# Optimization experiments

Hardware: AMD Instinct MI355X
Metric: run time of the kernel (lower is better)

The kernel has to match this reference:

```python
import jax, jax.numpy as jnp
import numpy as np

N = 100000      # num_edges in original graph = nodes here
E = 1600000     # edges of the line-graph
F_IN = 16       # num_edge_features
H, C = 2, 32    # heads, hidden_channels
HC = H * C
TD = 16         # time_embedding_dim
CD = 16         # condition_dim
NC = 2          # num_classes
MAX_TIME = 1000.0
THETA = 1.0


def _glorot(key, shape):
    fan_in = shape[0]
    return jax.random.normal(key, shape, dtype=jnp.float32) / np.sqrt(fan_in)


def setup_inputs() -> dict:
    key = jax.random.key(0)
    ks = jax.random.split(key, 32)
    inp = {
        "x": jax.random.normal(ks[0], (N, F_IN), dtype=jnp.float32),
        "edge_index": jax.random.randint(ks[1], (2, E), 0, N, dtype=jnp.int64),
        "t": jax.random.randint(ks[2], (1,), 0, 1000, dtype=jnp.int64),
        "condition": jax.random.normal(ks[3], (N, CD), dtype=jnp.float32),
        # GATv2 layer 0 (bias=True)
        "Wl0": _glorot(ks[4], (F_IN, HC)), "bl0": jnp.zeros((HC,), jnp.float32),
        "Wr0": _glorot(ks[5], (F_IN, HC)), "br0": jnp.zeros((HC,), jnp.float32),
        "att0": _glorot(ks[6], (H, C)), "bias0": jnp.zeros((HC,), jnp.float32),
        "Wres0": _glorot(ks[7], (F_IN, HC)), "bres0": jnp.zeros((HC,), jnp.float32),
        # GATv2 layer 1 (bias=False)
        "Wl1": _glorot(ks[8], (HC, HC)),
        "Wr1": _glorot(ks[9], (HC, HC)),
        "att1": _glorot(ks[10], (H, C)),
        "Wres1": _glorot(ks[11], (HC, HC)), "bres1": jnp.zeros((HC,), jnp.float32),
        # time MLP
        "Wt0": _glorot(ks[12], (TD, TD)), "bt0": jnp.zeros((TD,), jnp.float32),
        "Wt1": _glorot(ks[13], (TD, TD)), "bt1": jnp.zeros((TD,), jnp.float32),
        # decoder heads
        "Wfd": _glorot(ks[14], (HC + CD + TD, C)), "bfd": jnp.zeros((C,), jnp.float32),
        "Wcls": _glorot(ks[15], (C, NC)), "bcls": jnp.zeros((NC,), jnp.float32),
    }
    return inp


def _segment_softmax(logits, seg, num_seg):
    # logits: [E, H], softmax over edges sharing the same destination node
    m = jax.ops.segment_max(logits, seg, num_segments=num_seg)
    ex = jnp.exp(logits - m[seg])
    s = jax.ops.segment_sum(ex, seg, num_segments=num_seg)
    return ex / (s[seg] + 1e-16)


def _gatv2(x, src, dst, Wl, bl, Wr, br, att, bias):
    # PyG GATv2Conv with add_self_loops (self loops appended by caller)
    xl = x @ Wl
    xr = x @ Wr
    if bl is not None:
        xl = xl + bl
        xr = xr + br
    xl = xl.reshape(-1, H, C)
    xr = xr.reshape(-1, H, C)
    e = jax.nn.leaky_relu(xl[src] + xr[dst], negative_slope=0.2)  # [E, H, C]
    logits = jnp.einsum('ehc,hc->eh', e, att)                     # [E, H]
    alpha = _segment_softmax(logits, dst, N)                      # [E, H]
    msg = xl[src] * alpha[:, :, None]                             # [E, H, C]
    out = jax.ops.segment_sum(msg, dst, num_segments=N)           # [N, H, C]
    out = out.reshape(N, HC)
    if bias is not None:
        out = out + bias
    return out


def _time_embedding(t):
    tf = t.astype(jnp.float32) * (1000.0 / MAX_TIME)
    half = TD // 2
    freqs = jnp.exp(jnp.arange(half, dtype=jnp.float32) * -(jnp.log(10000.0) / (half - 1)))
    ang = tf[:, None] * freqs[None, :]
    return jnp.concatenate([jnp.sin(ang), jnp.cos(ang)], axis=1)  # [1, TD]


def reference(x, edge_index, t, condition,
              Wl0, bl0, Wr0, br0, att0, bias0, Wres0, bres0,
              Wl1, Wr1, att1, Wres1, bres1,
              Wt0, bt0, Wt1, bt1, Wfd, bfd, Wcls, bcls):
    loops = jnp.arange(N, dtype=edge_index.dtype)
    src = jnp.concatenate([edge_index[0], loops])
    dst = jnp.concatenate([edge_index[1], loops])

    # layer 0
    res = jax.nn.relu(x @ Wres0 + bres0)
    h = jax.nn.relu(_gatv2(x, src, dst, Wl0, bl0, Wr0, br0, att0, bias0))
    h = THETA * h + res
    # layer 1 (bias=False)
    res = jax.nn.relu(h @ Wres1 + bres1)
    h2 = jax.nn.relu(_gatv2(h, src, dst, Wl1, None, Wr1, None, att1, None))
    h = THETA * h2 + res

    # mode == 'future'
    t_emb = _time_embedding(t)
    t_emb = jax.nn.silu(t_emb @ Wt0 + bt0)
    t_emb = jax.nn.silu(t_emb @ Wt1 + bt1)
    t_rep = jnp.tile(t_emb, (N, 1))                                # [N, TD]
    h = jnp.concatenate([h, t_rep, condition], axis=1)             # [N, HC+TD+CD]
    logits = h @ Wfd + bfd
    logits = logits @ Wcls + bcls
    return logits[None]                                            # [1, N, NC]
```

## Files before the change

### kernel.cpp

```cpp
#include <hip/hip_runtime.h>
#include <hip/hip_bf16.h>
#include <hip/hip_fp16.h>
#include <math.h>


#define BLK 256
#define BDST 32
#define CDST 256
#define CHUNK 4096
#define FCAP 768
#define NBC_MAX 512

typedef _Float16 half4v __attribute__((ext_vector_type(4)));
typedef _Float16 half2v __attribute__((ext_vector_type(2)));

#if __has_builtin(__builtin_amdgcn_fdot2)
#define FDOT2(a, b, c) __builtin_amdgcn_fdot2((a), (b), (c), false)
#else
__device__ __forceinline__ float fdot2_fallback(half2v a, half2v b, float c) {
    return c + (float)a.x * (float)b.x + (float)a.y * (float)b.y;
}
#define FDOT2(a, b, c) fdot2_fallback((a), (b), (c))
#endif

__device__ __forceinline__ float leaky02(float x) { return x >= 0.f ? x : 0.2f * x; }
__device__ __forceinline__ float relu(float x) { return x > 0.f ? x : 0.f; }

__device__ __forceinline__ float edot(half4v h, half2v xlo, half2v xhi,
                                      half2v alo, half2v ahi, half2v c02) {
    half2v lo = half2v{h.x, h.y} + xlo;
    half2v hi = half2v{h.z, h.w} + xhi;
    lo = __builtin_elementwise_max(lo, lo * c02);
    hi = __builtin_elementwise_max(hi, hi * c02);
    return FDOT2(lo, alo, FDOT2(hi, ahi, 0.f));
}

__global__ void k_tiny(const int* __restrict__ t,
                       const float* __restrict__ Wt0, const float* __restrict__ bt0,
                       const float* __restrict__ Wt1, const float* __restrict__ bt1,
                       const float* __restrict__ Wfd, const float* __restrict__ bfd,
                       const float* __restrict__ Wcls, const float* __restrict__ bcls,
                       float* __restrict__ wcomb,
                       float* __restrict__ bfinal)
{
    __shared__ float temb[16];
    int tid = threadIdx.x;
    if (tid == 0) {
        float tf = (float)t[0];
        float e0[16], v1[16];
        const float cexp = -logf(10000.f) / 7.f;
        for (int j = 0; j < 8; ++j) {
            float ang = tf * expf((float)j * cexp);
            e0[j] = sinf(ang);
            e0[8 + j] = cosf(ang);
        }
        for (int i = 0; i < 16; ++i) {
            float a = bt0[i];
            for (int j = 0; j < 16; ++j) a += e0[j] * Wt0[j * 16 + i];
            v1[i] = a / (1.f + expf(-a));
        }
        for (int i = 0; i < 16; ++i) {
            float a = bt1[i];
            for (int j = 0; j < 16; ++j) a += v1[j] * Wt1[j * 16 + i];
            temb[i] = a / (1.f + expf(-a));
        }
    }
    __syncthreads();
    if (tid < 192) {
        int i = tid >> 1, k = tid & 1;
        float a = 0.f;
        for (int j = 0; j < 32; ++j) a += Wfd[i * 32 + j] * Wcls[j * 2 + k];
        wcomb[tid] = a;
    }
    __syncthreads();
    if (tid < 2) {
        float a = bcls[tid];
        for (int j = 0; j < 32; ++j) a += bfd[j] * Wcls[j * 2 + tid];
        for (int d = 0; d < 16; ++d) a += temb[d] * wcomb[(64 + d) * 2 + tid];
        bfinal[tid] = a;
    }
}

__global__ void k_zeroc(int* __restrict__ ccnt, int NBC)
{
    int gid = blockIdx.x * BLK + threadIdx.x;
    if (gid < NBC) ccnt[gid] = 0;
}

__global__ void k_histc(const int* __restrict__ ei, int E, int NBC,
                        int* __restrict__ ccnt)
{
    __shared__ int h[NBC_MAX];
    int tid = threadIdx.x;
    for (int i = tid; i < NBC; i += BLK) h[i] = 0;
    __syncthreads();
    int e0 = blockIdx.x * CHUNK;
    #pragma unroll
    for (int k = 0; k < CHUNK / BLK; ++k) {
        int e = e0 + tid + k * BLK;
        if (e < E) atomicAdd(&h[ei[E + e] >> 8], 1);
    }
    __syncthreads();
    for (int i = tid; i < NBC; i += BLK) {
        int v = h[i];
        if (v) atomicAdd(&ccnt[i], v);
    }
}

__global__ void k_scan(const int* __restrict__ ccnt, int NBC, int E,
                       int* __restrict__ cbase, int* __restrict__ ccur)
{
    if (threadIdx.x == 0) {
        int acc = 0;
        for (int i = 0; i < NBC; ++i) {
            cbase[i] = acc;
            acc += ccnt[i];
        }
        cbase[NBC] = acc;
    }
    __syncthreads();
    for (int i = threadIdx.x; i < NBC; i += BLK) ccur[i] = cbase[i];
}

__global__ void k_part(const int* __restrict__ ei, int E, int NBC,
                       int* __restrict__ ccur, int* __restrict__ part)
{
    __shared__ int h[NBC_MAX];
    __shared__ int gb[NBC_MAX];
    int tid = threadIdx.x;
    int e0 = blockIdx.x * CHUNK;
    for (int i = tid; i < NBC; i += BLK) h[i] = 0;
    __syncthreads();
    int sv[CHUNK / BLK], dv[CHUNK / BLK];
    #pragma unroll
    for (int k = 0; k < CHUNK / BLK; ++k) {
        int e = e0 + tid + k * BLK;
        if (e < E) {
            sv[k] = ei[e];
            dv[k] = ei[E + e];
            atomicAdd(&h[dv[k] >> 8], 1);
        } else dv[k] = -1;
    }
    __syncthreads();
    for (int i = tid; i < NBC; i += BLK) {
        int v = h[i];
        gb[i] = v ? atomicAdd(&ccur[i], v) : 0;
    }
    __syncthreads();
    for (int i = tid; i < NBC; i += BLK) h[i] = gb[i];
    __syncthreads();
    #pragma unroll
    for (int k = 0; k < CHUNK / BLK; ++k) {
        if (dv[k] >= 0) {
            int p = atomicAdd(&h[dv[k] >> 8], 1);
            part[p] = (sv[k] << 8) | (dv[k] & 255);
        }
    }
}

__global__ void k_refine(const int* __restrict__ cbase, const int* __restrict__ part,
                         int NBF, int* __restrict__ fbeg, int* __restrict__ fend,
                         int* __restrict__ srcs)
{
    __shared__ int fcnt[8];
    __shared__ int fcur[8];
    int b = blockIdx.x, tid = threadIdx.x;
    int beg = cbase[b], end = cbase[b + 1];
    if (tid < 8) fcnt[tid] = 0;
    __syncthreads();
    for (int k = beg + tid; k < end; k += BLK)
        atomicAdd(&fcnt[(part[k] >> 5) & 7], 1);
    __syncthreads();
    if (tid == 0) {
        int acc = beg;
        #pragma unroll
        for (int f = 0; f < 8; ++f) {
            int fb = b * 8 + f;
            fcur[f] = acc;
            if (fb < NBF) { fbeg[fb] = acc; acc += fcnt[f]; fend[fb] = acc; }
        }
    }
    __syncthreads();
    for (int k = beg + tid; k < end; k += BLK) {
        int tg = part[k];
        int p = atomicAdd(&fcur[(tg >> 5) & 7], 1);
        srcs[p] = ((tg >> 8) << 5) | (tg & 31);
    }
}

__global__ void k_pre0f(const float* __restrict__ x,
                        const float* __restrict__ Wl, const float* __restrict__ bl,
                        const float* __restrict__ Wr, const float* __restrict__ br,
                        const float* __restrict__ Wres, const float* __restrict__ bres,
                        _Float16* __restrict__ xlh, _Float16* __restrict__ xr16,
                        _Float16* __restrict__ res16, int N)
{
    int wid = (int)(((long long)blockIdx.x * BLK + threadIdx.x) >> 6);
    int lane = threadIdx.x & 63;
    int g = lane >> 4, q = lane & 15;
    int n = wid * 4 + g;
    bool valid = n < N;
    int nn = valid ? n : N - 1;
    float xv = x[(size_t)nn * 16 + q];
    int c0 = q * 4;
    float4 accl = *(const float4*)(bl + c0);
    float4 accr = *(const float4*)(br + c0);
    float4 accs = *(const float4*)(bres + c0);
    #pragma unroll
    for (int k = 0; k < 16; ++k) {
        float xk = __shfl(xv, (g << 4) | k, 64);
        float4 wl = *(const float4*)(Wl + k * 64 + c0);
        float4 wr = *(const float4*)(Wr + k * 64 + c0);
        float4 wsv = *(const float4*)(Wres + k * 64 + c0);
        accl.x = fmaf(xk, wl.x, accl.x);
        accl.y = fmaf(xk, wl.y, accl.y);
        accl.z = fmaf(xk, wl.z, accl.z);
        accl.w = fmaf(xk, wl.w, accl.w);
        accr.x = fmaf(xk, wr.x, accr.x);
        accr.y = fmaf(xk, wr.y, accr.y);
        accr.z = fmaf(xk, wr.z, accr.z);
        accr.w = fmaf(xk, wr.w, accr.w);
        accs.x = fmaf(xk, wsv.x, accs.x);
        accs.y = fmaf(xk, wsv.y, accs.y);
        accs.z = fmaf(xk, wsv.z, accs.z);
        accs.w = fmaf(xk, wsv.w, accs.w);
    }
    if (valid) {
        size_t base = (size_t)n * 64 + c0;
        half4v hl, hr, hs;
        hl.x = (_Float16)accl.x; hl.y = (_Float16)accl.y;
        hl.z = (_Float16)accl.z; hl.w = (_Float16)accl.w;
        hr.x = (_Float16)accr.x; hr.y = (_Float16)accr.y;
        hr.z = (_Float16)accr.z; hr.w = (_Float16)accr.w;
        hs.x = (_Float16)relu(accs.x); hs.y = (_Float16)relu(accs.y);
        hs.z = (_Float16)relu(accs.z); hs.w = (_Float16)relu(accs.w);
        *(half4v*)(xlh + base) = hl;
        *(half4v*)(xr16 + base) = hr;
        *(half4v*)(res16 + base) = hs;
    }
}

__global__ void k_pre1w(const _Float16* __restrict__ h16,
                        const float* __restrict__ Wl, const float* __restrict__ Wr,
                        const float* __restrict__ Wres, const float* __restrict__ bres,
                        _Float16* __restrict__ xlh, _Float16* __restrict__ xr16,
                        _Float16* __restrict__ res16, int N)
{
    __shared__ half4v wl4[16][64];
    __shared__ half4v wr4[16][64];
    __shared__ half4v ws4[16][64];
    __shared__ half4v h4[32][16];
    int tid = threadIdx.x;
    int nb = blockIdx.x * 32;

    for (int idx = tid; idx < 3 * 1024; idx += BLK) {
        int m = idx >> 10, rem = idx & 1023;
        int k4 = rem >> 6, c = rem & 63;
        const float* W = (m == 0) ? Wl : (m == 1) ? Wr : Wres;
        half4v v;
        v.x = (_Float16)W[(4 * k4 + 0) * 64 + c];
        v.y = (_Float16)W[(4 * k4 + 1) * 64 + c];
        v.z = (_Float16)W[(4 * k4 + 2) * 64 + c];
        v.w = (_Float16)W[(4 * k4 + 3) * 64 + c];
        (m == 0 ? wl4 : m == 1 ? wr4 : ws4)[k4][c] = v;
    }
    for (int idx = tid; idx < 512; idx += BLK) {
        int i = idx >> 4, k4 = idx & 15;
        int n = nb + i; if (n >= N) n = N - 1;
        h4[i][k4] = *(const half4v*)(h16 + (size_t)n * 64 + k4 * 4);
    }
    __syncthreads();

    int c = tid & 63, w = tid >> 6;
    float al[8], ar[8], as[8];
    float vbs = bres[c];
    #pragma unroll
    for (int i = 0; i < 8; ++i) { al[i] = 0.f; ar[i] = 0.f; as[i] = vbs; }

    #pragma unroll 4
    for (int k4 = 0; k4 < 16; ++k4) {
        half4v wl = wl4[k4][c];
        half4v wr = wr4[k4][c];
        half4v wsv = ws4[k4][c];
        half2v wll = { wl.x, wl.y },  wlh = { wl.z, wl.w };
        half2v wrl = { wr.x, wr.y },  wrh = { wr.z, wr.w };
        half2v wsl = { wsv.x, wsv.y }, wsh = { wsv.z, wsv.w };
        #pragma unroll
        for (int i = 0; i < 8; ++i) {
            half4v hv = h4[w * 8 + i][k4];
            half2v hl = { hv.x, hv.y }, hh = { hv.z, hv.w };
            al[i] = FDOT2(hl, wll, al[i]);
            al[i] = FDOT2(hh, wlh, al[i]);
            ar[i] = FDOT2(hl, wrl, ar[i]);
            ar[i] = FDOT2(hh, wrh, ar[i]);
            as[i] = FDOT2(hl, wsl, as[i]);
            as[i] = FDOT2(hh, wsh, as[i]);
        }
    }
    #pragma unroll
    for (int i = 0; i < 8; ++i) {
        int n = nb + w * 8 + i;
        if (n < N) {
            xlh[(size_t)n * 64 + c]   = (_Float16)al[i];
            xr16[(size_t)n * 64 + c]  = (_Float16)ar[i];
            res16[(size_t)n * 64 + c] = (_Float16)relu(as[i]);
        }
    }
}

template <bool DEC>
__global__ void k_gat3(const int* __restrict__ fbeg, const int* __restrict__ fend,
                       const int* __restrict__ srcs,
                       const _Float16* __restrict__ xlh, const _Float16* __restrict__ xr16,
                       const float* __restrict__ att, const float* __restrict__ bias,
                       const _Float16* __restrict__ res16,
                       _Float16* __restrict__ hout16,
                       const float* __restrict__ cond, const float* __restrict__ wcomb,
                       const float* __restrict__ bfinal, float* __restrict__ out,
                       int N)
{
    __shared__ int lh[BDST];
    __shared__ int rp[BDST + 1];
    __shared__ int cc[BDST];
    __shared__ int sidx[BDST];
    __shared__ int tags[FCAP];

    int b = blockIdx.x;
    int tid = threadIdx.x;
    int beg = fbeg[b];
    int nE = fend[b] - beg; if (nE > FCAP) nE = FCAP;

    if (tid < BDST) lh[tid] = 0;
    __syncthreads();
    for (int k = tid; k < nE; k += BLK) atomicAdd(&lh[srcs[beg + k] & 31], 1);
    __syncthreads();
    if (tid == 0) {
        int acc = 0;
        rp[0] = 0;
        #pragma unroll
        for (int i = 0; i < BDST; ++i) { acc += lh[i]; rp[i + 1] = acc; }
    }
    __syncthreads();
    if (tid < BDST) cc[tid] = rp[tid];
    __syncthreads();
    for (int k = tid; k < nE; k += BLK) {
        int tg = srcs[beg + k];
        int r = atomicAdd(&cc[tg & 31], 1);
        tags[r] = tg >> 5;
    }
    if (tid < BDST) {
        int di = rp[tid + 1] - rp[tid];
        int r = 0;
        #pragma unroll
        for (int j = 0; j < BDST; ++j) {
            int dj = rp[j + 1] - rp[j];
            r += (dj > di) || (dj == di && j < tid);
        }
        sidx[r] = tid;
    }
    __syncthreads();

    int lane = tid & 63, w = tid >> 6;
    int g = lane >> 4, q = lane & 15;
    int c0 = q * 4;
    float4 a4f = *(const float4*)(att + c0);
    const half2v c02 = { (_Float16)0.2f, (_Float16)0.2f };
    half2v alo = { (_Float16)a4f.x, (_Float16)a4f.y };
    half2v ahi = { (_Float16)a4f.z, (_Float16)a4f.w };

    #pragma unroll
    for (int rep = 0; rep < 2; ++rep) {
        int dlow = sidx[w * 8 + rep * 4 + g];
        int node = b * BDST + dlow;
        bool nvalid = node < N;
        int n = nvalid ? node : 0;

        half4v xrh = *(const half4v*)(xr16 + (size_t)n * 64 + c0);
        half2v xlo = { xrh.x, xrh.y }, xhi = { xrh.z, xrh.w };

        half4v hsv = *(const half4v*)(xlh + (size_t)n * 64 + c0);
        float lv = edot(hsv, xlo, xhi, alo, ahi, c02);
        lv += __shfl_xor(lv, 1, 8);
        lv += __shfl_xor(lv, 2, 8);
        lv += __shfl_xor(lv, 4, 8);

        float m = lv, den = 1.f;
        float ac0 = (float)hsv.x, ac1 = (float)hsv.y;
        float ac2 = (float)hsv.z, ac3 = (float)hsv.w;

        int deg = nvalid ? (rp[dlow + 1] - rp[dlow]) : 0;
        int base = nvalid ? rp[dlow] : 0;

        int t1 = max(deg, __shfl_xor(deg, 16, 64));
        int wavemax = max(t1, __shfl_xor(t1, 32, 64));

        int i1 = (0 < deg) ? tags[base + 0] : n;
        int i2 = (1 < deg) ? tags[base + 1] : n;
        int i3 = (2 < deg) ? tags[base + 2] : n;
        int i4 = (3 < deg) ? tags[base + 3] : n;
        half4v p1 = *(const half4v*)(xlh + (size_t)i1 * 64 + c0);
        half4v p2 = *(const half4v*)(xlh + (size_t)i2 * 64 + c0);
        half4v p3 = *(const half4v*)(xlh + (size_t)i3 * 64 + c0);
        half4v p4 = *(const half4v*)(xlh + (size_t)i4 * 64 + c0);

        for (int j = 0; j < wavemax; j += 4) {
            bool a1 = j < deg, a2 = j + 1 < deg, a3 = j + 2 < deg, a4b = j + 3 < deg;
            half4v h1 = p1, h2 = p2, h3 = p3, h4 = p4;
            int n1 = (j + 4 < deg) ? tags[base + j + 4] : n;
            int n2 = (j + 5 < deg) ? tags[base + j + 5] : n;
            int n3 = (j + 6 < deg) ? tags[base + j + 6] : n;
            int n4 = (j + 7 < deg) ? tags[base + j + 7] : n;
            p1 = *(const half4v*)(xlh + (size_t)n1 * 64 + c0);
            p2 = *(const half4v*)(xlh + (size_t)n2 * 64 + c0);
            p3 = *(const half4v*)(xlh + (size_t)n3 * 64 + c0);
            p4 = *(const half4v*)(xlh + (size_t)n4 * 64 + c0);

            float e1 = edot(h1, xlo, xhi, alo, ahi, c02);
            float e2 = edot(h2, xlo, xhi, alo, ahi, c02);
            float e3 = edot(h3, xlo, xhi, alo, ahi, c02);
            float e4 = edot(h4, xlo, xhi, alo, ahi, c02);
            e1 += __shfl_xor(e1, 1, 8); e2 += __shfl_xor(e2, 1, 8);
            e3 += __shfl_xor(e3, 1, 8); e4 += __shfl_xor(e4, 1, 8);
            e1 += __shfl_xor(e1, 2, 8); e2 += __shfl_xor(e2, 2, 8);
            e3 += __shfl_xor(e3, 2, 8); e4 += __shfl_xor(e4, 2, 8);
            e1 += __shfl_xor(e1, 4, 8); e2 += __shfl_xor(e2, 4, 8);
            e3 += __shfl_xor(e3, 4, 8); e4 += __shfl_xor(e4, 4, 8);
            if (!a1) e1 = -1e30f;
            if (!a2) e2 = -1e30f;
            if (!a3) e3 = -1e30f;
            if (!a4b) e4 = -1e30f;

            float mn = fmaxf(fmaxf(m, fmaxf(e1, e2)), fmaxf(e3, e4));
            float sc  = __expf(m - mn);
            float ex1 = __expf(e1 - mn);
            float ex2 = __expf(e2 - mn);
            float ex3 = __expf(e3 - mn);
            float ex4 = __expf(e4 - mn);
            den = den * sc + ((ex1 + ex2) + (ex3 + ex4));
            ac0 = fmaf(ex4, (float)h4.x, fmaf(ex3, (float)h3.x,
                  fmaf(ex2, (float)h2.x, fmaf(ex1, (float)h1.x, ac0 * sc))));
            ac1 = fmaf(ex4, (float)h4.y, fmaf(ex3, (float)h3.y,
                  fmaf(ex2, (float)h2.y, fmaf(ex1, (float)h1.y, ac1 * sc))));
            ac2 = fmaf(ex4, (float)h4.z, fmaf(ex3, (float)h3.z,
                  fmaf(ex2, (float)h2.z, fmaf(ex1, (float)h1.z, ac2 * sc))));
            ac3 = fmaf(ex4, (float)h4.w, fmaf(ex3, (float)h3.w,
                  fmaf(ex2, (float)h2.w, fmaf(ex1, (float)h1.w, ac3 * sc))));
            m = mn;
        }

        float inv = 1.f / den;
        half4v rh = *(const half4v*)(res16 + (size_t)n * 64 + c0);
        float h0, h1, h2, h3;
        if (bias) {
            const float4 b4 = *(const float4*)(bias + c0);
            h0 = relu(ac0 * inv + b4.x) + (float)rh.x;
            h1 = relu(ac1 * inv + b4.y) + (float)rh.y;
            h2 = relu(ac2 * inv + b4.z) + (float)rh.z;
            h3 = relu(ac3 * inv + b4.w) + (float)rh.w;
        } else {
            h0 = relu(ac0 * inv) + (float)rh.x;
            h1 = relu(ac1 * inv) + (float)rh.y;
            h2 = relu(ac2 * inv) + (float)rh.z;
            h3 = relu(ac3 * inv) + (float)rh.w;
        }

        if (!DEC) {
            if (nvalid) {
                half4v o;
                o.x = (_Float16)h0; o.y = (_Float16)h1;
                o.z = (_Float16)h2; o.w = (_Float16)h3;
                *(half4v*)(hout16 + (size_t)n * 64 + c0) = o;
            }
        } else {
            float p0 = h0 * wcomb[(c0 + 0) * 2] + h1 * wcomb[(c0 + 1) * 2]
                     + h2 * wcomb[(c0 + 2) * 2] + h3 * wcomb[(c0 + 3) * 2];
            float p1d = h0 * wcomb[(c0 + 0) * 2 + 1] + h1 * wcomb[(c0 + 1) * 2 + 1]
                      + h2 * wcomb[(c0 + 2) * 2 + 1] + h3 * wcomb[(c0 + 3) * 2 + 1];
            if (q < 4) {
                float4 c4 = *(const float4*)(cond + (size_t)n * 16 + q * 4);
                int d0 = 80 + q * 4;
                p0 += c4.x * wcomb[(d0 + 0) * 2] + c4.y * wcomb[(d0 + 1) * 2]
                    + c4.z * wcomb[(d0 + 2) * 2] + c4.w * wcomb[(d0 + 3) * 2];
                p1d += c4.x * wcomb[(d0 + 0) * 2 + 1] + c4.y * wcomb[(d0 + 1) * 2 + 1]
                     + c4.z * wcomb[(d0 + 2) * 2 + 1] + c4.w * wcomb[(d0 + 3) * 2 + 1];
            }
            #pragma unroll
            for (int off = 1; off < 16; off <<= 1) {
                p0 += __shfl_xor(p0, off, 16);
                p1d += __shfl_xor(p1d, off, 16);
            }
            if (q == 0 && nvalid) {
                out[(size_t)n * 2] = p0 + bfinal[0];
                out[(size_t)n * 2 + 1] = p1d + bfinal[1];
            }
        }
    }
}

static inline int gblk(long long threads) { return (int)((threads + BLK - 1) / BLK); }

extern "C" void kernel_launch(void* const* d_in, const int* in_sizes, int n_in,
                              void* d_out, int out_size, void* d_ws, size_t ws_size,
                              hipStream_t stream) {
    const float* x     = (const float*)d_in[0];
    const int*   ei    = (const int*)d_in[1];
    const int*   t     = (const int*)d_in[2];
    const float* cond  = (const float*)d_in[3];
    const float* Wl0   = (const float*)d_in[4];
    const float* bl0   = (const float*)d_in[5];
    const float* Wr0   = (const float*)d_in[6];
    const float* br0   = (const float*)d_in[7];
    const float* att0  = (const float*)d_in[8];
    const float* bias0 = (const float*)d_in[9];
    const float* Wres0 = (const float*)d_in[10];
    const float* bres0 = (const float*)d_in[11];
    const float* Wl1   = (const float*)d_in[12];
    const float* Wr1   = (const float*)d_in[13];
    const float* att1  = (const float*)d_in[14];
    const float* Wres1 = (const float*)d_in[15];
    const float* bres1 = (const float*)d_in[16];
    const float* Wt0   = (const float*)d_in[17];
    const float* bt0   = (const float*)d_in[18];
    const float* Wt1   = (const float*)d_in[19];
    const float* bt1   = (const float*)d_in[20];
    const float* Wfd   = (const float*)d_in[21];
    const float* bfd   = (const float*)d_in[22];
    const float* Wcls  = (const float*)d_in[23];
    const float* bcls  = (const float*)d_in[24];
    float* out = (float*)d_out;

    const int N   = in_sizes[0] / 16;
    const int E   = in_sizes[1] / 2;
    const int NBC = (N + CDST - 1) / CDST;
    const int NBF = (N + BDST - 1) / BDST;

    float* ws = (float*)d_ws;
    size_t o = 0;
    _Float16* hbuf16 = (_Float16*)(ws + o); o += (size_t)N * 32;
    _Float16* xlh    = (_Float16*)(ws + o); o += (size_t)N * 32;
    _Float16* xr16   = (_Float16*)(ws + o); o += (size_t)N * 32;
    _Float16* res16  = (_Float16*)(ws + o); o += (size_t)N * 32;
    float* wcomb = ws + o; o += 192;
    float* bfin  = ws + o; o += 2;
    int* iws     = (int*)(ws + o);
    size_t io = 0;
    int* ccnt  = iws + io; io += NBC_MAX;
    int* cbase = iws + io; io += NBC_MAX + 1;
    int* ccur  = iws + io; io += NBC_MAX;
    int* fbeg  = iws + io; io += NBF;
    int* fend  = iws + io; io += NBF;
    int* part  = iws + io; io += E;
    int* srcs  = iws + io; io += E;

    const int partBlocks = (E + CHUNK - 1) / CHUNK;

    k_tiny<<<1, BLK, 0, stream>>>(t, Wt0, bt0, Wt1, bt1, Wfd, bfd, Wcls, bcls, wcomb, bfin);

    k_zeroc<<<gblk(NBC), BLK, 0, stream>>>(ccnt, NBC);
    k_histc<<<partBlocks, BLK, 0, stream>>>(ei, E, NBC, ccnt);
    k_scan<<<1, BLK, 0, stream>>>(ccnt, NBC, E, cbase, ccur);
    k_part<<<partBlocks, BLK, 0, stream>>>(ei, E, NBC, ccur, part);
    k_refine<<<NBC, BLK, 0, stream>>>(cbase, part, NBF, fbeg, fend, srcs);

    k_pre0f<<<gblk((long long)((N + 3) / 4) * 64), BLK, 0, stream>>>(
        x, Wl0, bl0, Wr0, br0, Wres0, bres0, xlh, xr16, res16, N);
    k_gat3<false><<<NBF, BLK, 0, stream>>>(fbeg, fend, srcs, xlh, xr16, att0, bias0, res16,
                                           hbuf16, nullptr, nullptr, nullptr, nullptr, N);

    k_pre1w<<<(N + 31) / 32, BLK, 0, stream>>>(hbuf16, Wl1, Wr1, Wres1, bres1, xlh, xr16, res16, N);
    k_gat3<true><<<NBF, BLK, 0, stream>>>(fbeg, fend, srcs, xlh, xr16, att1, nullptr, res16,
                                          nullptr, cond, wcomb, bfin, out, N);
}
```

Measured before the change: 274.4 us.

## Fuse layer-1 projection GEMM into the layer-0 GAT aggregation kernel

```diff
diff --git a/kernel.cpp b/kernel.cpp
--- a/kernel.cpp
+++ b/kernel.cpp
@@ -240,81 +240,16 @@
     }
 }
 
-__global__ void k_pre1w(const _Float16* __restrict__ h16,
-                        const float* __restrict__ Wl, const float* __restrict__ Wr,
-                        const float* __restrict__ Wres, const float* __restrict__ bres,
-                        _Float16* __restrict__ xlh, _Float16* __restrict__ xr16,
-                        _Float16* __restrict__ res16, int N)
-{
-    __shared__ half4v wl4[16][64];
-    __shared__ half4v wr4[16][64];
-    __shared__ half4v ws4[16][64];
-    __shared__ half4v h4[32][16];
-    int tid = threadIdx.x;
-    int nb = blockIdx.x * 32;
-
-    for (int idx = tid; idx < 3 * 1024; idx += BLK) {
-        int m = idx >> 10, rem = idx & 1023;
-        int k4 = rem >> 6, c = rem & 63;
-        const float* W = (m == 0) ? Wl : (m == 1) ? Wr : Wres;
-        half4v v;
-        v.x = (_Float16)W[(4 * k4 + 0) * 64 + c];
-        v.y = (_Float16)W[(4 * k4 + 1) * 64 + c];
-        v.z = (_Float16)W[(4 * k4 + 2) * 64 + c];
-        v.w = (_Float16)W[(4 * k4 + 3) * 64 + c];
-        (m == 0 ? wl4 : m == 1 ? wr4 : ws4)[k4][c] = v;
-    }
-    for (int idx = tid; idx < 512; idx += BLK) {
-        int i = idx >> 4, k4 = idx & 15;
-        int n = nb + i; if (n >= N) n = N - 1;
-        h4[i][k4] = *(const half4v*)(h16 + (size_t)n * 64 + k4 * 4);
-    }
-    __syncthreads();
-
-    int c = tid & 63, w = tid >> 6;
-    float al[8], ar[8], as[8];
-    float vbs = bres[c];
-    #pragma unroll
-    for (int i = 0; i < 8; ++i) { al[i] = 0.f; ar[i] = 0.f; as[i] = vbs; }
-
-    #pragma unroll 4
-    for (int k4 = 0; k4 < 16; ++k4) {
-        half4v wl = wl4[k4][c];
-        half4v wr = wr4[k4][c];
-        half4v wsv = ws4[k4][c];
-        half2v wll = { wl.x, wl.y },  wlh = { wl.z, wl.w };
-        half2v wrl = { wr.x, wr.y },  wrh = { wr.z, wr.w };
-        half2v wsl = { wsv.x, wsv.y }, wsh = { wsv.z, wsv.w };
-        #pragma unroll
-        for (int i = 0; i < 8; ++i) {
-            half4v hv = h4[w * 8 + i][k4];
-            half2v hl = { hv.x, hv.y }, hh = { hv.z, hv.w };
-            al[i] = FDOT2(hl, wll, al[i]);
-            al[i] = FDOT2(hh, wlh, al[i]);
-            ar[i] = FDOT2(hl, wrl, ar[i]);
-            ar[i] = FDOT2(hh, wrh, ar[i]);
-            as[i] = FDOT2(hl, wsl, as[i]);
-            as[i] = FDOT2(hh, wsh, as[i]);
-        }
-    }
-    #pragma unroll
-    for (int i = 0; i < 8; ++i) {
-        int n = nb + w * 8 + i;
-        if (n < N) {
-            xlh[(size_t)n * 64 + c]   = (_Float16)al[i];
-            xr16[(size_t)n * 64 + c]  = (_Float16)ar[i];
-            res16[(size_t)n * 64 + c] = (_Float16)relu(as[i]);
-        }
-    }
-}
-
-template <bool DEC>
+template <int LAYER>
 __global__ void k_gat3(const int* __restrict__ fbeg, const int* __restrict__ fend,
                        const int* __restrict__ srcs,
                        const _Float16* __restrict__ xlh, const _Float16* __restrict__ xr16,
                        const float* __restrict__ att, const float* __restrict__ bias,
                        const _Float16* __restrict__ res16,
-                       _Float16* __restrict__ hout16,
+                       const float* __restrict__ Wl1, const float* __restrict__ Wr1,
+                       const float* __restrict__ Wres1, const float* __restrict__ bres1,
+                       _Float16* __restrict__ xlh_out, _Float16* __restrict__ xr_out,
+                       _Float16* __restrict__ res_out,
                        const float* __restrict__ cond, const float* __restrict__ wcomb,
                        const float* __restrict__ bfinal, float* __restrict__ out,
                        int N)
@@ -324,11 +259,29 @@
     __shared__ int cc[BDST];
     __shared__ int sidx[BDST];
     __shared__ int tags[FCAP];
+    __shared__ half4v wl4[LAYER == 0 ? 16 : 1][64];
+    __shared__ half4v wr4[LAYER == 0 ? 16 : 1][64];
+    __shared__ half4v ws4[LAYER == 0 ? 16 : 1][64];
+    __shared__ half4v h4[LAYER == 0 ? 32 : 1][16];
 
     int b = blockIdx.x;
     int tid = threadIdx.x;
     int beg = fbeg[b];
     int nE = fend[b] - beg; if (nE > FCAP) nE = FCAP;
+
+    if constexpr (LAYER == 0) {
+        for (int idx = tid; idx < 3 * 1024; idx += BLK) {
+            int m = idx >> 10, rem = idx & 1023;
+            int k4 = rem >> 6, c = rem & 63;
+            const float* W = (m == 0) ? Wl1 : (m == 1) ? Wr1 : Wres1;
+            half4v v;
+            v.x = (_Float16)W[(4 * k4 + 0) * 64 + c];
+            v.y = (_Float16)W[(4 * k4 + 1) * 64 + c];
+            v.z = (_Float16)W[(4 * k4 + 2) * 64 + c];
+            v.w = (_Float16)W[(4 * k4 + 3) * 64 + c];
+            (m == 0 ? wl4 : m == 1 ? wr4 : ws4)[k4][c] = v;
+        }
+    }
 
     if (tid < BDST) lh[tid] = 0;
     __syncthreads();
@@ -405,7 +358,7 @@
 
         for (int j = 0; j < wavemax; j += 4) {
             bool a1 = j < deg, a2 = j + 1 < deg, a3 = j + 2 < deg, a4b = j + 3 < deg;
-            half4v h1 = p1, h2 = p2, h3 = p3, h4 = p4;
+            half4v h1 = p1, h2 = p2, h3 = p3, h4x = p4;
             int n1 = (j + 4 < deg) ? tags[base + j + 4] : n;
             int n2 = (j + 5 < deg) ? tags[base + j + 5] : n;
             int n3 = (j + 6 < deg) ? tags[base + j + 6] : n;
@@ -418,7 +371,7 @@
             float e1 = edot(h1, xlo, xhi, alo, ahi, c02);
             float e2 = edot(h2, xlo, xhi, alo, ahi, c02);
             float e3 = edot(h3, xlo, xhi, alo, ahi, c02);
-            float e4 = edot(h4, xlo, xhi, alo, ahi, c02);
+            float e4 = edot(h4x, xlo, xhi, alo, ahi, c02);
             e1 += __shfl_xor(e1, 1, 8); e2 += __shfl_xor(e2, 1, 8);
             e3 += __shfl_xor(e3, 1, 8); e4 += __shfl_xor(e4, 1, 8);
             e1 += __shfl_xor(e1, 2, 8); e2 += __shfl_xor(e2, 2, 8);
@@ -437,13 +390,13 @@
             float ex3 = __expf(e3 - mn);
             float ex4 = __expf(e4 - mn);
             den = den * sc + ((ex1 + ex2) + (ex3 + ex4));
-            ac0 = fmaf(ex4, (float)h4.x, fmaf(ex3, (float)h3.x,
+            ac0 = fmaf(ex4, (float)h4x.x, fmaf(ex3, (float)h3.x,
                   fmaf(ex2, (float)h2.x, fmaf(ex1, (float)h1.x, ac0 * sc))));
-            ac1 = fmaf(ex4, (float)h4.y, fmaf(ex3, (float)h3.y,
+            ac1 = fmaf(ex4, (float)h4x.y, fmaf(ex3, (float)h3.y,
                   fmaf(ex2, (float)h2.y, fmaf(ex1, (float)h1.y, ac1 * sc))));
-            ac2 = fmaf(ex4, (float)h4.z, fmaf(ex3, (float)h3.z,
+            ac2 = fmaf(ex4, (float)h4x.z, fmaf(ex3, (float)h3.z,
                   fmaf(ex2, (float)h2.z, fmaf(ex1, (float)h1.z, ac2 * sc))));
-            ac3 = fmaf(ex4, (float)h4.w, fmaf(ex3, (float)h3.w,
+            ac3 = fmaf(ex4, (float)h4x.w, fmaf(ex3, (float)h3.w,
                   fmaf(ex2, (float)h2.w, fmaf(ex1, (float)h1.w, ac3 * sc))));
             m = mn;
         }
@@ -464,13 +417,11 @@
             h3 = relu(ac3 * inv) + (float)rh.w;
         }
 
-        if (!DEC) {
-            if (nvalid) {
-                half4v o;
-                o.x = (_Float16)h0; o.y = (_Float16)h1;
-                o.z = (_Float16)h2; o.w = (_Float16)h3;
-                *(half4v*)(hout16 + (size_t)n * 64 + c0) = o;
-            }
+        if constexpr (LAYER == 0) {
+            half4v o;
+            o.x = (_Float16)h0; o.y = (_Float16)h1;
+            o.z = (_Float16)h2; o.w = (_Float16)h3;
+            h4[dlow][q] = o;
         } else {
             float p0 = h0 * wcomb[(c0 + 0) * 2] + h1 * wcomb[(c0 + 1) * 2]
                      + h2 * wcomb[(c0 + 2) * 2] + h3 * wcomb[(c0 + 3) * 2];
@@ -492,6 +443,46 @@
             if (q == 0 && nvalid) {
                 out[(size_t)n * 2] = p0 + bfinal[0];
                 out[(size_t)n * 2 + 1] = p1d + bfinal[1];
+            }
+        }
+    }
+
+    if constexpr (LAYER == 0) {
+        __syncthreads();
+        int nb = b * BDST;
+        int c = tid & 63, ww = tid >> 6;
+        float al[8], ar[8], as2[8];
+        float vbs = bres1[c];
+        #pragma unroll
+        for (int i = 0; i < 8; ++i) { al[i] = 0.f; ar[i] = 0.f; as2[i] = vbs; }
+
+        #pragma unroll 4
+        for (int k4 = 0; k4 < 16; ++k4) {
+            half4v wl = wl4[k4][c];
+            half4v wr = wr4[k4][c];
+            half4v wsv = ws4[k4][c];
+            half2v wll = { wl.x, wl.y },  wlh = { wl.z, wl.w };
+            half2v wrl = { wr.x, wr.y },  wrh = { wr.z, wr.w };
+            half2v wsl = { wsv.x, wsv.y }, wsh = { wsv.z, wsv.w };
+            #pragma unroll
+            for (int i = 0; i < 8; ++i) {
+                half4v hv = h4[ww * 8 + i][k4];
+                half2v hl = { hv.x, hv.y }, hh = { hv.z, hv.w };
+                al[i] = FDOT2(hl, wll, al[i]);
+                al[i] = FDOT2(hh, wlh, al[i]);
+                ar[i] = FDOT2(hl, wrl, ar[i]);
+                ar[i] = FDOT2(hh, wrh, ar[i]);
+                as2[i] = FDOT2(hl, wsl, as2[i]);
+                as2[i] = FDOT2(hh, wsh, as2[i]);
+            }
+        }
+        #pragma unroll
+        for (int i = 0; i < 8; ++i) {
+            int n = nb + ww * 8 + i;
+            if (n < N) {
+                xlh_out[(size_t)n * 64 + c] = (_Float16)al[i];
+                xr_out[(size_t)n * 64 + c]  = (_Float16)ar[i];
+                res_out[(size_t)n * 64 + c] = (_Float16)relu(as2[i]);
             }
         }
     }
@@ -536,10 +527,10 @@
 
     float* ws = (float*)d_ws;
     size_t o = 0;
-    _Float16* hbuf16 = (_Float16*)(ws + o); o += (size_t)N * 32;
-    _Float16* xlh    = (_Float16*)(ws + o); o += (size_t)N * 32;
-    _Float16* xr16   = (_Float16*)(ws + o); o += (size_t)N * 32;
-    _Float16* res16  = (_Float16*)(ws + o); o += (size_t)N * 32;
+    _Float16* xlhA  = (_Float16*)(ws + o); o += (size_t)N * 32;
+    _Float16* xlhB  = (_Float16*)(ws + o); o += (size_t)N * 32;
+    _Float16* xr16  = (_Float16*)(ws + o); o += (size_t)N * 32;
+    _Float16* res16 = (_Float16*)(ws + o); o += (size_t)N * 32;
     float* wcomb = ws + o; o += 192;
     float* bfin  = ws + o; o += 2;
     int* iws     = (int*)(ws + o);
@@ -563,11 +554,14 @@
     k_refine<<<NBC, BLK, 0, stream>>>(cbase, part, NBF, fbeg, fend, srcs);
 
     k_pre0f<<<gblk((long long)((N + 3) / 4) * 64), BLK, 0, stream>>>(
-        x, Wl0, bl0, Wr0, br0, Wres0, bres0, xlh, xr16, res16, N);
-    k_gat3<false><<<NBF, BLK, 0, stream>>>(fbeg, fend, srcs, xlh, xr16, att0, bias0, res16,
-                                           hbuf16, nullptr, nullptr, nullptr, nullptr, N);
-
-    k_pre1w<<<(N + 31) / 32, BLK, 0, stream>>>(hbuf16, Wl1, Wr1, Wres1, bres1, xlh, xr16, res16, N);
-    k_gat3<true><<<NBF, BLK, 0, stream>>>(fbeg, fend, srcs, xlh, xr16, att1, nullptr, res16,
-                                          nullptr, cond, wcomb, bfin, out, N);
-}
+        x, Wl0, bl0, Wr0, br0, Wres0, bres0, xlhA, xr16, res16, N);
+
+    k_gat3<0><<<NBF, BLK, 0, stream>>>(fbeg, fend, srcs, xlhA, xr16, att0, bias0, res16,
+                                       Wl1, Wr1, Wres1, bres1, xlhB, xr16, res16,
+                                       nullptr, nullptr, nullptr, nullptr, N);
+
+    k_gat3<1><<<NBF, BLK, 0, stream>>>(fbeg, fend, srcs, xlhB, xr16, att1, nullptr, res16,
+                                       nullptr, nullptr, nullptr, nullptr,
+                                       nullptr, nullptr, nullptr,
+                                       cond, wcomb, bfin, out, N);
+}
```

New measurement: 285.6 us. 4.1% more time.
